# Kernel tuning notes

Measured on AMD Instinct MI355X. Metric: run time of the kernel, lower is better.

## Reference

```python
import jax, jax.numpy as jnp
import numpy as np

D_MODEL = 512
NUM_HEADS = 8
D_K = D_MODEL // NUM_HEADS  # 64
LN_EPS = 1e-5


def setup_inputs() -> dict:
    key = jax.random.key(0)
    ks = jax.random.split(key, 6)
    B, S, D = 8, 1024, D_MODEL
    scale = 1.0 / np.sqrt(D)
    return {
        "query": jax.random.normal(ks[0], (B, S, D), jnp.float32),
        "key": jax.random.normal(ks[1], (B, S, D), jnp.float32),
        "value": jax.random.normal(ks[2], (B, S, D), jnp.float32),
        "Wq": jax.random.normal(ks[3], (D, D), jnp.float32) * scale,
        "bq": jnp.zeros((D,), jnp.float32),
        "Wk": jax.random.normal(ks[4], (D, D), jnp.float32) * scale,
        "bk": jnp.zeros((D,), jnp.float32),
        "Wo": jax.random.normal(ks[5], (D, D * NUM_HEADS), jnp.float32) * (1.0 / np.sqrt(D * NUM_HEADS)),
        "bo": jnp.zeros((D,), jnp.float32),
        "gamma": jnp.ones((D,), jnp.float32),
        "beta": jnp.zeros((D,), jnp.float32),
    }


def reference(query, key, value, Wq, bq, Wk, bk, Wo, bo, gamma, beta):
    B, S, D = value.shape
    h, dk = NUM_HEADS, D_K
    # QK projections -> [B, h, S, dk]
    q = (query @ Wq.T + bq).reshape(B, S, h, dk).transpose(0, 2, 1, 3)
    k = (key @ Wk.T + bk).reshape(B, S, h, dk).transpose(0, 2, 1, 3)
    # scaled dot-product scores [B, h, Sq, Sk]
    scores = jnp.einsum("bhqd,bhkd->bhqk", q, k) / jnp.sqrt(jnp.asarray(dk, q.dtype))
    attn = jax.nn.softmax(scores, axis=-1)
    # value broadcast across heads: value is [B, Sk, D] -> per-head output [B, h, Sq, D]
    x = jnp.einsum("bhqk,bkd->bhqd", attn, value)
    # concat heads -> [B, Sq, h*D], output projection back to D
    x = x.transpose(0, 2, 1, 3).reshape(B, S, h * D)
    x = x @ Wo.T + bo
    # residual + LayerNorm (dropout = identity in eval)
    y = value + x
    mu = jnp.mean(y, axis=-1, keepdims=True)
    var = jnp.var(y, axis=-1, keepdims=True)
    out = (y - mu) * jax.lax.rsqrt(var + LN_EPS) * gamma + beta
    return out, attn
```

## Files before the change

### kernel.cpp

```cpp
#include <hip/hip_runtime.h>
#include <hip/hip_bf16.h>

#define B_ 8
#define S_ 1024
#define D_ 512
#define H_ 8
#define DK_ 64
#define HD_ 4096

typedef __attribute__((ext_vector_type(8))) short bf16x8;
typedef __attribute__((ext_vector_type(4))) float f32x4;

static __device__ __forceinline__ unsigned short f2bf(float f) {
    unsigned u = __float_as_uint(f);
    unsigned r = (u + 0x7fffu + ((u >> 16) & 1u)) >> 16;
    return (unsigned short)r;
}

static __device__ __forceinline__ void gload16(const unsigned short* g, unsigned short* l) {
    __builtin_amdgcn_global_load_lds(
        (const __attribute__((address_space(1))) void*)g,
        (__attribute__((address_space(3))) void*)l, 16, 0, 0);
}

static __device__ __forceinline__ int plidx(int ql, int k) {
    return ql * 1024 + ((((k >> 3) ^ (ql & 7))) << 3) + (k & 7);
}

__global__ __launch_bounds__(256) void cvt_kernel(
    const float* __restrict__ src, unsigned short* __restrict__ dst)
{
    const size_t i = ((size_t)blockIdx.x * 256 + threadIdx.x) * 4;
    float4 v = *(const float4*)&src[i];
    ushort4 u = { f2bf(v.x), f2bf(v.y), f2bf(v.z), f2bf(v.w) };
    *(ushort4*)&dst[i] = u;
}

__global__ __launch_bounds__(256) void cvt2_kernel(
    const float* __restrict__ s0, unsigned short* __restrict__ d0,
    const float* __restrict__ s1, unsigned short* __restrict__ d1, int nb0)
{
    const bool first = (int)blockIdx.x < nb0;
    const float* s = first ? s0 : s1;
    unsigned short* d = first ? d0 : d1;
    const int bid = first ? blockIdx.x : blockIdx.x - nb0;
    const size_t i = ((size_t)bid * 256 + threadIdx.x) * 4;
    float4 v = *(const float4*)&s[i];
    ushort4 u = { f2bf(v.x), f2bf(v.y), f2bf(v.z), f2bf(v.w) };
    *(ushort4*)&d[i] = u;
}

__global__ __launch_bounds__(256) void vt_kernel(
    const float* __restrict__ V, unsigned short* __restrict__ Vt)
{
    __shared__ float tile[32][33];
    const int b = blockIdx.z, s0 = blockIdx.x * 32, e0 = blockIdx.y * 32;
    const int t = threadIdx.x;
    const int r = t >> 3, c4 = (t & 7) * 4;
    float4 v = *(const float4*)&V[((size_t)b * S_ + s0 + r) * D_ + e0 + c4];
    tile[r][c4 + 0] = v.x; tile[r][c4 + 1] = v.y;
    tile[r][c4 + 2] = v.z; tile[r][c4 + 3] = v.w;
    __syncthreads();
    ushort4 u;
    u.x = f2bf(tile[c4 + 0][r]); u.y = f2bf(tile[c4 + 1][r]);
    u.z = f2bf(tile[c4 + 2][r]); u.w = f2bf(tile[c4 + 3][r]);
    *(ushort4*)&Vt[((size_t)b * D_ + e0 + r) * S_ + s0 + c4] = u;
}

template<int KDIM, int TN, int MODE>
__global__ __launch_bounds__(256) void gemm_t(
    const unsigned short* __restrict__ A, const unsigned short* __restrict__ Bw,
    const float* __restrict__ bias, const float* __restrict__ Vres,
    void* __restrict__ Out, float scale)
{
    constexpr int NB = 512 / TN;
    constexpr int CF = TN / 32;
    const int o = blockIdx.x;
    const int cpx = gridDim.x / 8;
    const int nb = (o % 8) * cpx + o / 8;
    const int m0 = (nb / NB) * 128;
    const int n0 = (nb % NB) * TN;

    __shared__ __align__(16) unsigned short As[2][128 * 32];
    __shared__ __align__(16) unsigned short Bs[2][TN * 32];

    const int t = threadIdx.x;
    const int wave = t >> 6, lane = t & 63;
    const int wr = wave >> 1, wc = wave & 1;
    const int lr = lane & 15, g = lane >> 4;
    const int gx = (g ^ (lr & 3)) << 3;

    f32x4 acc[4][CF];
    #pragma unroll
    for (int r = 0; r < 4; ++r)
        #pragma unroll
        for (int c = 0; c < CF; ++c) acc[r][c] = (f32x4){0.f, 0.f, 0.f, 0.f};

    const int sub = lane >> 2;
    const int cb  = (((lane & 3) ^ (sub & 3)) << 3);

    auto stage = [&](int buf, int k0) {
        #pragma unroll
        for (int s = 0; s < 2; ++s) {
            const int chunk = s * 4 + wave;
            const int row = chunk * 16 + sub;
            gload16(&A[(size_t)(m0 + row) * KDIM + k0 + cb], &As[buf][chunk * 512]);
        }
        #pragma unroll
        for (int s = 0; s < TN / 64; ++s) {
            const int chunk = s * 4 + wave;
            const int row = chunk * 16 + sub;
            gload16(&Bw[(size_t)(n0 + row) * KDIM + k0 + cb], &Bs[buf][chunk * 512]);
        }
    };
    auto compute = [&](int cur) {
        bf16x8 af[4], bfr[CF];
        #pragma unroll
        for (int r = 0; r < 4; ++r)
            af[r] = *(const bf16x8*)&As[cur][(wr * 64 + r * 16 + lr) * 32 + gx];
        #pragma unroll
        for (int c = 0; c < CF; ++c)
            bfr[c] = *(const bf16x8*)&Bs[cur][(wc * (TN / 2) + c * 16 + lr) * 32 + gx];
        __builtin_amdgcn_s_setprio(1);
        #pragma unroll
        for (int c = 0; c < CF; ++c)
            #pragma unroll
            for (int r = 0; r < 4; ++r)
                acc[r][c] = __builtin_amdgcn_mfma_f32_16x16x32_bf16(af[r], bfr[c], acc[r][c], 0, 0, 0);
        __builtin_amdgcn_s_setprio(0);
    };

    const int NT = KDIM / 32;
    stage(0, 0);
    __syncthreads();
    int cur = 0;
    for (int tt = 0; tt < NT - 1; ++tt) {
        stage(cur ^ 1, (tt + 1) * 32);
        compute(cur);
        __syncthreads();
        cur ^= 1;
    }
    compute(cur);

    float bn[CF];
    #pragma unroll
    for (int c = 0; c < CF; ++c) bn[c] = bias[n0 + wc * (TN / 2) + c * 16 + lr];

    #pragma unroll
    for (int r = 0; r < 4; ++r) {
        #pragma unroll
        for (int c = 0; c < CF; ++c) {
            const int n = n0 + wc * (TN / 2) + c * 16 + lr;
            #pragma unroll
            for (int i = 0; i < 4; ++i) {
                const int m = m0 + wr * 64 + r * 16 + g * 4 + i;
                if constexpr (MODE == 0) {
                    const int srow = m & 1023, bb = m >> 10;
                    const int h = n >> 6, dk = n & 63;
                    ((unsigned short*)Out)[(((size_t)(bb * H_ + h)) * S_ + srow) * DK_ + dk] =
                        f2bf((acc[r][c][i] + bn[c]) * scale);
                } else {
                    const size_t oo = (size_t)m * D_ + n;
                    ((float*)Out)[oo] = acc[r][c][i] + bn[c] + Vres[oo];
                }
            }
        }
    }
}

__global__ __launch_bounds__(1024, 4) void fused_attn(
    const unsigned short* __restrict__ Qbf,
    const unsigned short* __restrict__ Kbf,
    const unsigned short* __restrict__ Vt,
    float* __restrict__ attn,
    unsigned short* __restrict__ AV)
{
    const int o = blockIdx.x;
    const int nb = (o & 7) * 128 + (o >> 3);
    const int bh = nb >> 4;
    const int q0 = (nb & 15) * 64;
    const int b = bh >> 3, h = bh & 7;
    const unsigned short* Qb = Qbf + (size_t)bh * S_ * DK_;
    const unsigned short* Kb = Kbf + (size_t)bh * S_ * DK_;
    const unsigned short* Vb = Vt + (size_t)b * D_ * S_;
    float* outp = attn + ((size_t)bh << 20);

    __shared__ unsigned short PL[64 * 1024];
    __shared__ float redm[64][16];
    __shared__ float rowm[64];

    const int t = threadIdx.x;
    const int wave = t >> 6, lane = t & 63;
    const int wcol = wave * 64;
    const int lr = lane & 15;
    const int g  = lane >> 4;

    f32x4 acc[4][4];
    #pragma unroll
    for (int r = 0; r < 4; ++r)
        #pragma unroll
        for (int c = 0; c < 4; ++c) acc[r][c] = (f32x4){0.f, 0.f, 0.f, 0.f};

    #pragma unroll
    for (int kk = 0; kk < 2; ++kk) {
        bf16x8 af[4];
        #pragma unroll
        for (int r = 0; r < 4; ++r)
            af[r] = *(const bf16x8*)&Kb[(size_t)(wcol + r * 16 + lr) * DK_ + kk * 32 + g * 8];
        bf16x8 qf[4];
        #pragma unroll
        for (int c = 0; c < 4; ++c)
            qf[c] = *(const bf16x8*)&Qb[(size_t)(q0 + c * 16 + lr) * DK_ + kk * 32 + g * 8];
        __builtin_amdgcn_s_setprio(1);
        #pragma unroll
        for (int r = 0; r < 4; ++r)
            #pragma unroll
            for (int c = 0; c < 4; ++c)
                acc[r][c] = __builtin_amdgcn_mfma_f32_16x16x32_bf16(af[r], qf[c], acc[r][c], 0, 0, 0);
        __builtin_amdgcn_s_setprio(0);
    }

    float mloc[4];
    #pragma unroll
    for (int c = 0; c < 4; ++c) {
        float m = acc[0][c][0];
        #pragma unroll
        for (int r = 0; r < 4; ++r)
            #pragma unroll
            for (int i = 0; i < 4; ++i) m = fmaxf(m, acc[r][c][i]);
        m = fmaxf(m, __shfl_xor(m, 16));
        m = fmaxf(m, __shfl_xor(m, 32));
        mloc[c] = m;
    }
    if (lane < 16) {
        #pragma unroll
        for (int c = 0; c < 4; ++c) redm[c * 16 + lane][wave] = mloc[c];
    }
    __syncthreads();
    if (t < 64) {
        float m = redm[t][0];
        #pragma unroll
        for (int w = 1; w < 16; ++w) m = fmaxf(m, redm[t][w]);
        rowm[t] = m;
    }
    __syncthreads();
    float sloc[4];
    #pragma unroll
    for (int c = 0; c < 4; ++c) {
        const float m = rowm[c * 16 + lr];
        float s = 0.f;
        #pragma unroll
        for (int r = 0; r < 4; ++r)
            #pragma unroll
            for (int i = 0; i < 4; ++i) {
                float p = __expf(acc[r][c][i] - m);
                acc[r][c][i] = p;
                s += p;
            }
        s += __shfl_xor(s, 16);
        s += __shfl_xor(s, 32);
        sloc[c] = s;
    }
    __syncthreads();
    if (lane < 16) {
        #pragma unroll
        for (int c = 0; c < 4; ++c) redm[c * 16 + lane][wave] = sloc[c];
    }
    __syncthreads();
    if (t < 64) {
        float s = redm[t][0];
        #pragma unroll
        for (int w = 1; w < 16; ++w) s += redm[t][w];
        rowm[t] = 1.0f / s;
    }
    __syncthreads();

    #pragma unroll
    for (int c = 0; c < 4; ++c) {
        const int ql = c * 16 + lr;
        const float ri = rowm[ql];
        #pragma unroll
        for (int r = 0; r < 4; ++r) {
            f32x4 v = acc[r][c];
            v[0] *= ri; v[1] *= ri; v[2] *= ri; v[3] *= ri;
            const int k = wcol + r * 16 + g * 4;
            unsigned p01 = (unsigned)f2bf(v[0]) | ((unsigned)f2bf(v[1]) << 16);
            unsigned p23 = (unsigned)f2bf(v[2]) | ((unsigned)f2bf(v[3]) << 16);
            uint2 pk = { p01, p23 };
            *(uint2*)&PL[plidx(ql, k)] = pk;
        }
    }
    __syncthreads();

    {
        const int arow = t >> 4;
        const int akb  = (t & 15) * 8;
        float* rowp = outp + ((size_t)(q0 + arow) << 10);
        #pragma unroll
        for (int j = 0; j < 8; ++j) {
            const int k = akb + j * 128;
            uint4 u = *(const uint4*)&PL[plidx(arow, k)];
            f32x4 f0, f1;
            f0[0] = __uint_as_float((u.x & 0xffffu) << 16);
            f0[1] = __uint_as_float(u.x & 0xffff0000u);
            f0[2] = __uint_as_float((u.y & 0xffffu) << 16);
            f0[3] = __uint_as_float(u.y & 0xffff0000u);
            f1[0] = __uint_as_float((u.z & 0xffffu) << 16);
            f1[1] = __uint_as_float(u.z & 0xffff0000u);
            f1[2] = __uint_as_float((u.w & 0xffffu) << 16);
            f1[3] = __uint_as_float(u.w & 0xffff0000u);
            __builtin_nontemporal_store(f0, (f32x4*)&rowp[k]);
            __builtin_nontemporal_store(f1, (f32x4*)&rowp[k + 4]);
        }
    }

    const int we = wave * 32;
    f32x4 accv[4][2];
    #pragma unroll
    for (int r = 0; r < 4; ++r)
        #pragma unroll
        for (int c = 0; c < 2; ++c) accv[r][c] = (f32x4){0.f, 0.f, 0.f, 0.f};

    const unsigned short* vp0 = Vb + (size_t)(we + lr) * S_ + g * 8;
    const unsigned short* vp1 = Vb + (size_t)(we + 16 + lr) * S_ + g * 8;
    bf16x8 vf0 = *(const bf16x8*)vp0;
    bf16x8 vf1 = *(const bf16x8*)vp1;

    for (int k0 = 0; k0 < S_; k0 += 32) {
        bf16x8 nv0, nv1;
        const int kn = k0 + 32;
        if (kn < S_) {
            nv0 = *(const bf16x8*)(vp0 + kn);
            nv1 = *(const bf16x8*)(vp1 + kn);
        }
        bf16x8 pa[4];
        #pragma unroll
        for (int r = 0; r < 4; ++r)
            pa[r] = *(const bf16x8*)&PL[plidx(r * 16 + lr, k0 + g * 8)];
        __builtin_amdgcn_s_setprio(1);
        #pragma unroll
        for (int r = 0; r < 4; ++r)
            accv[r][0] = __builtin_amdgcn_mfma_f32_16x16x32_bf16(pa[r], vf0, accv[r][0], 0, 0, 0);
        #pragma unroll
        for (int r = 0; r < 4; ++r)
            accv[r][1] = __builtin_amdgcn_mfma_f32_16x16x32_bf16(pa[r], vf1, accv[r][1], 0, 0, 0);
        __builtin_amdgcn_s_setprio(0);
        if (kn < S_) { vf0 = nv0; vf1 = nv1; }
    }

    #pragma unroll
    for (int r = 0; r < 4; ++r) {
        #pragma unroll
        for (int c = 0; c < 2; ++c) {
            const int e = we + c * 16 + lr;
            #pragma unroll
            for (int i = 0; i < 4; ++i) {
                const int row = q0 + r * 16 + g * 4 + i;
                AV[((size_t)(b * S_ + row)) * HD_ + h * D_ + e] = f2bf(accv[r][c][i]);
            }
        }
    }
}

__global__ __launch_bounds__(256) void ln_kernel(
    float* __restrict__ Y, const float* __restrict__ gamma,
    const float* __restrict__ beta)
{
    const int lane = threadIdx.x & 63;
    const int wave = threadIdx.x >> 6;
    const size_t row = (size_t)blockIdx.x * 4 + wave;
    float* p = Y + row * D_;
    float4 v0 = *(float4*)&p[lane * 4];
    float4 v1 = *(float4*)&p[256 + lane * 4];
    float s = v0.x + v0.y + v0.z + v0.w + v1.x + v1.y + v1.z + v1.w;
    float q = v0.x * v0.x + v0.y * v0.y + v0.z * v0.z + v0.w * v0.w +
              v1.x * v1.x + v1.y * v1.y + v1.z * v1.z + v1.w * v1.w;
    #pragma unroll
    for (int m = 1; m < 64; m <<= 1) {
        s += __shfl_xor(s, m);
        q += __shfl_xor(q, m);
    }
    const float mu  = s * (1.f / 512.f);
    const float var = q * (1.f / 512.f) - mu * mu;
    const float r = rsqrtf(var + 1e-5f);
    const float4 g0 = *(const float4*)&gamma[lane * 4];
    const float4 g1 = *(const float4*)&gamma[256 + lane * 4];
    const float4 b0 = *(const float4*)&beta[lane * 4];
    const float4 b1 = *(const float4*)&beta[256 + lane * 4];
    v0.x = (v0.x - mu) * r * g0.x + b0.x;
    v0.y = (v0.y - mu) * r * g0.y + b0.y;
    v0.z = (v0.z - mu) * r * g0.z + b0.z;
    v0.w = (v0.w - mu) * r * g0.w + b0.w;
    v1.x = (v1.x - mu) * r * g1.x + b1.x;
    v1.y = (v1.y - mu) * r * g1.y + b1.y;
    v1.z = (v1.z - mu) * r * g1.z + b1.z;
    v1.w = (v1.w - mu) * r * g1.w + b1.w;
    *(float4*)&p[lane * 4] = v0;
    *(float4*)&p[256 + lane * 4] = v1;
}

extern "C" void kernel_launch(void* const* d_in, const int* in_sizes, int n_in,
                              void* d_out, int out_size, void* d_ws, size_t ws_size,
                              hipStream_t stream)
{
    const float* query = (const float*)d_in[0];
    const float* key   = (const float*)d_in[1];
    const float* value = (const float*)d_in[2];
    const float* Wq    = (const float*)d_in[3];
    const float* bq    = (const float*)d_in[4];
    const float* Wk    = (const float*)d_in[5];
    const float* bk    = (const float*)d_in[6];
    const float* Wo    = (const float*)d_in[7];
    const float* bo    = (const float*)d_in[8];
    const float* gamma = (const float*)d_in[9];
    const float* beta  = (const float*)d_in[10];

    float* out  = (float*)d_out;
    float* attn = out + (size_t)B_ * S_ * D_;
    char*  attnB = (char*)attn;

    char* ws = (char*)d_ws;
    unsigned short* AV   = (unsigned short*)ws;
    unsigned short* Vt   = (unsigned short*)(ws + ((size_t)64 << 20));
    unsigned short* Wobf = (unsigned short*)(ws + ((size_t)72 << 20));
    unsigned short* Qbf  = (unsigned short*)d_out;
    unsigned short* Kbf  = (unsigned short*)d_out + ((size_t)4 << 20);
    unsigned short* Xq   = (unsigned short*)(attnB + ((size_t)200 << 20));
    unsigned short* Xk   = (unsigned short*)(attnB + ((size_t)210 << 20));
    unsigned short* Wqbf = (unsigned short*)(attnB + ((size_t)220 << 20));
    unsigned short* Wkbf = (unsigned short*)(attnB + ((size_t)221 << 20));

    cvt2_kernel<<<8192, 256, 0, stream>>>(query, Xq, key, Xk, 4096);
    cvt2_kernel<<<512,  256, 0, stream>>>(Wq, Wqbf, Wk, Wkbf, 256);
    cvt_kernel<<<2048, 256, 0, stream>>>(Wo, Wobf);
    vt_kernel<<<dim3(32, 16, 8), 256, 0, stream>>>(value, Vt);
    gemm_t<512, 64, 0><<<512, 256, 0, stream>>>(Xq, Wqbf, bq, nullptr, (void*)Qbf, 0.125f);
    gemm_t<512, 64, 0><<<512, 256, 0, stream>>>(Xk, Wkbf, bk, nullptr, (void*)Kbf, 1.0f);
    fused_attn<<<1024, 1024, 0, stream>>>(Qbf, Kbf, Vt, attn, AV);
    gemm_t<4096, 64, 1><<<512, 256, 0, stream>>>(AV, Wobf, bo, value, (void*)out, 0.f);
    ln_kernel<<<2048, 256, 0, stream>>>(out, gamma, beta);
}
```

Baseline: 349.1 us.

## Stage AV output through LDS for coalesced stores and read head-major AV in GEMM

The attention kernel now writes its per-head AV tile to LDS and then stores it in wide 16-byte coalesced chunks, in a [B,H,S,D] layout instead of the scattered 2-byte stores into [B,S,H*D]. The output-projection GEMM loader (MODE != 0) remaps its A addresses to read this head-major layout. The attention-probability writeback is reorganised so each wave streams whole rows, and the bf16 packing uses the v_cvt_pk_bf16_f32 instruction. The aim is to cut uncoalesced global traffic, at the cost of extra barriers and LDS reuse after the PV loop.

```diff
diff --git a/kernel.cpp b/kernel.cpp
--- a/kernel.cpp
+++ b/kernel.cpp
@@ -104,7 +104,15 @@
         for (int s = 0; s < 2; ++s) {
             const int chunk = s * 4 + wave;
             const int row = chunk * 16 + sub;
-            gload16(&A[(size_t)(m0 + row) * KDIM + k0 + cb], &As[buf][chunk * 512]);
+            if constexpr (MODE == 0) {
+                gload16(&A[(size_t)(m0 + row) * KDIM + k0 + cb], &As[buf][chunk * 512]);
+            } else {
+                const int m = m0 + row;
+                const int bb = m >> 10, ss = m & 1023;
+                const int h = k0 >> 9;
+                gload16(&A[(((size_t)(bb * H_ + h)) * S_ + ss) * D_ + (k0 & 511) + cb],
+                        &As[buf][chunk * 512]);
+            }
         }
         #pragma unroll
         for (int s = 0; s < TN / 64; ++s) {
@@ -179,7 +187,7 @@
     const int nb = (o & 7) * 128 + (o >> 3);
     const int bh = nb >> 4;
     const int q0 = (nb & 15) * 64;
-    const int b = bh >> 3, h = bh & 7;
+    const int b = bh >> 3;
     const unsigned short* Qb = Qbf + (size_t)bh * S_ * DK_;
     const unsigned short* Kb = Kbf + (size_t)bh * S_ * DK_;
     const unsigned short* Vb = Vt + (size_t)b * D_ * S_;
@@ -284,34 +292,44 @@
             f32x4 v = acc[r][c];
             v[0] *= ri; v[1] *= ri; v[2] *= ri; v[3] *= ri;
             const int k = wcol + r * 16 + g * 4;
-            unsigned p01 = (unsigned)f2bf(v[0]) | ((unsigned)f2bf(v[1]) << 16);
-            unsigned p23 = (unsigned)f2bf(v[2]) | ((unsigned)f2bf(v[3]) << 16);
+            unsigned p01, p23;
+            asm("v_cvt_pk_bf16_f32 %0, %1, %2" : "=v"(p01) : "v"(v[0]), "v"(v[1]));
+            asm("v_cvt_pk_bf16_f32 %0, %1, %2" : "=v"(p23) : "v"(v[2]), "v"(v[3]));
             uint2 pk = { p01, p23 };
             *(uint2*)&PL[plidx(ql, k)] = pk;
         }
     }
     __syncthreads();
 
-    {
-        const int arow = t >> 4;
-        const int akb  = (t & 15) * 8;
-        float* rowp = outp + ((size_t)(q0 + arow) << 10);
-        #pragma unroll
-        for (int j = 0; j < 8; ++j) {
-            const int k = akb + j * 128;
-            uint4 u = *(const uint4*)&PL[plidx(arow, k)];
-            f32x4 f0, f1;
-            f0[0] = __uint_as_float((u.x & 0xffffu) << 16);
-            f0[1] = __uint_as_float(u.x & 0xffff0000u);
-            f0[2] = __uint_as_float((u.y & 0xffffu) << 16);
-            f0[3] = __uint_as_float(u.y & 0xffff0000u);
-            f1[0] = __uint_as_float((u.z & 0xffffu) << 16);
-            f1[1] = __uint_as_float(u.z & 0xffff0000u);
-            f1[2] = __uint_as_float((u.w & 0xffffu) << 16);
-            f1[3] = __uint_as_float(u.w & 0xffff0000u);
-            __builtin_nontemporal_store(f0, (f32x4*)&rowp[k]);
-            __builtin_nontemporal_store(f1, (f32x4*)&rowp[k + 4]);
-        }
+    #pragma unroll
+    for (int jj = 0; jj < 4; ++jj) {
+        const int row = wave * 4 + jj;
+        const int ps = lane ^ (row & 7);
+        float* rowp = outp + ((size_t)(q0 + row) << 10);
+        uint4 u0 = *(const uint4*)&PL[row * 1024 + (ps << 3)];
+        uint4 u1 = *(const uint4*)&PL[row * 1024 + ((64 + ps) << 3)];
+        f32x4 f0, f1, f2, f3;
+        f0[0] = __uint_as_float((u0.x & 0xffffu) << 16);
+        f0[1] = __uint_as_float(u0.x & 0xffff0000u);
+        f0[2] = __uint_as_float((u0.y & 0xffffu) << 16);
+        f0[3] = __uint_as_float(u0.y & 0xffff0000u);
+        f1[0] = __uint_as_float((u0.z & 0xffffu) << 16);
+        f1[1] = __uint_as_float(u0.z & 0xffff0000u);
+        f1[2] = __uint_as_float((u0.w & 0xffffu) << 16);
+        f1[3] = __uint_as_float(u0.w & 0xffff0000u);
+        f2[0] = __uint_as_float((u1.x & 0xffffu) << 16);
+        f2[1] = __uint_as_float(u1.x & 0xffff0000u);
+        f2[2] = __uint_as_float((u1.y & 0xffffu) << 16);
+        f2[3] = __uint_as_float(u1.y & 0xffff0000u);
+        f3[0] = __uint_as_float((u1.z & 0xffffu) << 16);
+        f3[1] = __uint_as_float(u1.z & 0xffff0000u);
+        f3[2] = __uint_as_float((u1.w & 0xffffu) << 16);
+        f3[3] = __uint_as_float(u1.w & 0xffff0000u);
+        const int k0f = lane * 8;
+        __builtin_nontemporal_store(f0, (f32x4*)&rowp[k0f]);
+        __builtin_nontemporal_store(f1, (f32x4*)&rowp[k0f + 4]);
+        __builtin_nontemporal_store(f2, (f32x4*)&rowp[512 + k0f]);
+        __builtin_nontemporal_store(f3, (f32x4*)&rowp[512 + k0f + 4]);
     }
 
     const int we = wave * 32;
@@ -348,16 +366,28 @@
         if (kn < S_) { vf0 = nv0; vf1 = nv1; }
     }
 
-    #pragma unroll
-    for (int r = 0; r < 4; ++r) {
+    __syncthreads();
+    unsigned short* PL2 = PL;
+    #pragma unroll
+    for (int r = 0; r < 4; ++r)
         #pragma unroll
         for (int c = 0; c < 2; ++c) {
             const int e = we + c * 16 + lr;
             #pragma unroll
             for (int i = 0; i < 4; ++i) {
-                const int row = q0 + r * 16 + g * 4 + i;
-                AV[((size_t)(b * S_ + row)) * HD_ + h * D_ + e] = f2bf(accv[r][c][i]);
+                const int row = r * 16 + g * 4 + i;
+                PL2[row * 520 + e] = f2bf(accv[r][c][i]);
             }
+        }
+    __syncthreads();
+    {
+        const int row = t >> 4;
+        unsigned short* avp = AV + ((size_t)bh * S_ + q0 + row) * D_;
+        #pragma unroll
+        for (int j = 0; j < 4; ++j) {
+            const int e0 = (t & 15) * 8 + j * 128;
+            uint4 u = *(const uint4*)&PL2[row * 520 + e0];
+            *(uint4*)&avp[e0] = u;
         }
     }
 }
```

Result: slower. 366.3 us (+4.9%).
